# Kernel tuning notes

Measured on AMD Instinct MI355X. Metric: run time of the kernel, lower is better.

Reference implementation:

```python
import jax, jax.numpy as jnp
import numpy as np

B, T, I, H, O = 65536, 50, 2, 20, 2
P_DROP = 0.2


def setup_inputs() -> dict:
    key = jax.random.key(0)
    ks = jax.random.split(key, 8)
    s = 1.0 / np.sqrt(H)  # torch nn.RNN / nn.Linear uniform init bound
    u = lambda k, shape: jax.random.uniform(k, shape, jnp.float32, -s, s)
    x = jax.random.normal(ks[0], (B, T, I), jnp.float32)
    W_ih = u(ks[1], (H, I))
    W_hh = u(ks[2], (H, H))
    b_ih = u(ks[3], (H,))
    b_hh = u(ks[4], (H,))
    W_out = u(ks[5], (O, H))
    b_out = u(ks[6], (O,))
    # MC-dropout mask (training-mode dropout, inverted scaling), fixed for determinism
    keep = jax.random.uniform(ks[7], (B, T, H)) >= P_DROP
    drop_mask = keep.astype(jnp.float32) / (1.0 - P_DROP)
    return {"x": x, "W_ih": W_ih, "W_hh": W_hh, "b_ih": b_ih, "b_hh": b_hh,
            "W_out": W_out, "b_out": b_out, "drop_mask": drop_mask}


def reference(x, W_ih, W_hh, b_ih, b_hh, W_out, b_out, drop_mask):
    # Precompute input projection for all timesteps in one big GEMM: [B,T,H]
    xp = jnp.einsum('bti,hi->bth', x, W_ih) + b_ih + b_hh

    def step(h, xt):  # h: [B,H], xt: [B,H]
        h_new = jnp.tanh(xt + h @ W_hh.T)
        return h_new, h_new

    h0 = jnp.zeros((x.shape[0], W_hh.shape[0]), x.dtype)
    _, hs = jax.lax.scan(step, h0, jnp.swapaxes(xp, 0, 1))  # hs: [T,B,H]
    r_out = jnp.swapaxes(hs, 0, 1)  # [B,T,H]
    out = (r_out * drop_mask) @ W_out.T + b_out  # [B,T,O]
    return out
```

## Files before the change

kernel.cpp:

```cpp
#include <hip/hip_runtime.h>

#ifndef __has_builtin
#define __has_builtin(x) 0
#endif

#if __has_builtin(__builtin_amdgcn_exp2f)
#define EXP2F(x) __builtin_amdgcn_exp2f(x)
#else
#define EXP2F(x) exp2f(x)
#endif

#if __has_builtin(__builtin_amdgcn_rcpf)
#define RCPF(x) __builtin_amdgcn_rcpf(x)
#else
#define RCPF(x) (1.0f / (x))
#endif

namespace {

constexpr int kB = 65536;
constexpr int kT = 50;
constexpr int kI = 2;
constexpr int kH = 20;
constexpr int kO = 2;

__device__ __forceinline__ float fast_tanh(float v) {
    const float p = EXP2F(v * 2.8853900817779268f);
    return fmaf(-2.0f, RCPF(p + 1.0f), 1.0f);
}

#if __has_builtin(__builtin_amdgcn_mov_dpp)
template <int CTRL>
__device__ __forceinline__ float fqp(float v) {
    return __int_as_float(
        __builtin_amdgcn_mov_dpp(__float_as_int(v), CTRL, 0xF, 0xF, true));
}
#else
template <int CTRL>
__device__ __forceinline__ float fqp(float v) {
    constexpr int d = (CTRL == 0xB1) ? 1 : (CTRL == 0x4E) ? 2 : 3;
    return __shfl_xor(v, d);
}
#endif

__global__ __launch_bounds__(256)
__attribute__((amdgpu_waves_per_eu(2, 3)))
void dprnn_kernel(
    const float* __restrict__ x, const float* __restrict__ W_ih,
    const float* __restrict__ W_hh, const float* __restrict__ b_ih,
    const float* __restrict__ b_hh, const float* __restrict__ W_out,
    const float* __restrict__ b_out, const float* __restrict__ mask,
    float* __restrict__ out)
{
    const int tid = blockIdx.x * 256 + threadIdx.x;
    const int g   = tid >> 2;
    const int sub = tid & 3;
    const int gl  = threadIdx.x >> 2;

    __shared__ __align__(16) float lout[64 * kT * kO];

    float w[5][5][4];
    float wi0[5], wi1[5], bia[5], wo0[5], wo1[5];
#pragma unroll
    for (int i = 0; i < 5; ++i) {
        const int row = 4 * i + sub;
#pragma unroll
        for (int r = 0; r < 5; ++r) {
#pragma unroll
            for (int d = 0; d < 4; ++d) {
                w[i][r][d] = W_hh[row * kH + 4 * r + (sub ^ d)];
            }
        }
        wi0[i] = W_ih[row * kI + 0];
        wi1[i] = W_ih[row * kI + 1];
        bia[i] = b_ih[row] + b_hh[row];
        wo0[i] = W_out[0 * kH + row];
        wo1[i] = W_out[1 * kH + row];
    }
    const float bo0 = b_out[0];
    const float bo1 = b_out[1];

    float h[5] = {0.f, 0.f, 0.f, 0.f, 0.f};

    const float* xp = x    + (size_t)g * (kT * kI);
    const float* mp = mask + (size_t)g * (kT * kH) + sub;

    auto step = [&](const float m[5], float x0, float x1, int t) {
        float acc[5];
#pragma unroll
        for (int i = 0; i < 5; ++i)
            acc[i] = fmaf(wi0[i], x0, fmaf(wi1[i], x1, bia[i]));
#pragma unroll
        for (int r = 0; r < 5; ++r) {
            const float v0 = h[r];
            const float v1 = fqp<0xB1>(h[r]);
            const float v2 = fqp<0x4E>(h[r]);
            const float v3 = fqp<0x1B>(h[r]);
#pragma unroll
            for (int i = 0; i < 5; ++i) {
                acc[i] = fmaf(w[i][r][0], v0, acc[i]);
                acc[i] = fmaf(w[i][r][1], v1, acc[i]);
                acc[i] = fmaf(w[i][r][2], v2, acc[i]);
                acc[i] = fmaf(w[i][r][3], v3, acc[i]);
            }
        }
        float p0 = 0.f, p1 = 0.f;
#pragma unroll
        for (int i = 0; i < 5; ++i) {
            const float hn = fast_tanh(acc[i]);
            h[i] = hn;
            const float dm = hn * m[i];
            p0 = fmaf(dm, wo0[i], p0);
            p1 = fmaf(dm, wo1[i], p1);
        }
        p0 += fqp<0xB1>(p0);
        p0 += fqp<0x4E>(p0);
        p1 += fqp<0xB1>(p1);
        p1 += fqp<0x4E>(p1);
        if (sub == 0) {
            *reinterpret_cast<float2*>(&lout[gl * (kT * kO) + t * kO]) =
                make_float2(p0 + bo0, p1 + bo1);
        }
    };

    float m0[5], m1[5];
#pragma unroll
    for (int r = 0; r < 5; ++r) m0[r] = mp[0 * kH + 4 * r];
#pragma unroll
    for (int r = 0; r < 5; ++r) m1[r] = mp[1 * kH + 4 * r];
    float4 xq = *reinterpret_cast<const float4*>(xp);

    for (int tb = 0; tb < kT - 2; tb += 2) {
        float n0[5], n1[5];
        const float* mq = mp + (tb + 2) * kH;
#pragma unroll
        for (int r = 0; r < 5; ++r) n0[r] = mq[4 * r];
#pragma unroll
        for (int r = 0; r < 5; ++r) n1[r] = mq[kH + 4 * r];
        const float4 xq_n =
            *reinterpret_cast<const float4*>(xp + (tb + 2) * kI);

        step(m0, xq.x, xq.y, tb);
        step(m1, xq.z, xq.w, tb + 1);

#pragma unroll
        for (int r = 0; r < 5; ++r) { m0[r] = n0[r]; m1[r] = n1[r]; }
        xq = xq_n;
    }
    step(m0, xq.x, xq.y, kT - 2);
    step(m1, xq.z, xq.w, kT - 1);

    __syncthreads();
    const int k = threadIdx.x;
    float* ob = out + (size_t)blockIdx.x * (64 * kT * kO);
#pragma unroll
    for (int it = 0; it < 6; ++it) {
        const int idx = it * 1024 + k * 4;
        const float4 v = *reinterpret_cast<const float4*>(&lout[idx]);
        *reinterpret_cast<float4*>(ob + idx) = v;
    }
    {
        const int idx = 6144 + k;
        ob[idx] = lout[idx];
    }
}

}

extern "C" void kernel_launch(void* const* d_in, const int* in_sizes, int n_in,
                              void* d_out, int out_size, void* d_ws, size_t ws_size,
                              hipStream_t stream) {
    const float* x     = (const float*)d_in[0];
    const float* W_ih  = (const float*)d_in[1];
    const float* W_hh  = (const float*)d_in[2];
    const float* b_ih  = (const float*)d_in[3];
    const float* b_hh  = (const float*)d_in[4];
    const float* W_out = (const float*)d_in[5];
    const float* b_out = (const float*)d_in[6];
    const float* mask  = (const float*)d_in[7];
    float* out = (float*)d_out;

    const int threads = kB * 4;
    dim3 block(256);
    dim3 grid(threads / 256);
    dprnn_kernel<<<grid, block, 0, stream>>>(x, W_ih, W_hh, b_ih, b_hh,
                                             W_out, b_out, mask, out);
}
```

Before: 87.37 us.

## Stage dropout mask chunks into LDS with coalesced global_load_lds and stream outputs

```diff
diff --git a/kernel.cpp b/kernel.cpp
--- a/kernel.cpp
+++ b/kernel.cpp
@@ -14,6 +14,12 @@
 #define RCPF(x) __builtin_amdgcn_rcpf(x)
 #else
 #define RCPF(x) (1.0f / (x))
+#endif
+
+#if __has_builtin(__builtin_amdgcn_global_load_lds)
+#define USE_GLOAD_LDS 1
+#else
+#define USE_GLOAD_LDS 0
 #endif
 
 namespace {
@@ -23,6 +29,14 @@
 constexpr int kI = 2;
 constexpr int kH = 20;
 constexpr int kO = 2;
+constexpr int kCT = 5;
+constexpr int kNC = 10;
+constexpr int kGB = 64;
+
+#if USE_GLOAD_LDS
+typedef const __attribute__((address_space(1))) void* gas_ptr_t;
+typedef __attribute__((address_space(3))) void* las_ptr_t;
+#endif
 
 __device__ __forceinline__ float fast_tanh(float v) {
     const float p = EXP2F(v * 2.8853900817779268f);
@@ -52,12 +66,16 @@
     const float* __restrict__ b_out, const float* __restrict__ mask,
     float* __restrict__ out)
 {
-    const int tid = blockIdx.x * 256 + threadIdx.x;
-    const int g   = tid >> 2;
-    const int sub = tid & 3;
-    const int gl  = threadIdx.x >> 2;
-
-    __shared__ __align__(16) float lout[64 * kT * kO];
+    __shared__ __align__(16) float sm[kGB * kCT * kH + kGB * kCT * kO];
+    float* lds_m = sm;
+    float* lds_o = sm + kGB * kCT * kH;
+
+    const int tidx = threadIdx.x;
+    const int gl   = tidx >> 2;
+    const int sub  = tidx & 3;
+    const int Wv   = tidx >> 6;
+    const int lane = tidx & 63;
+    const size_t g0 = (size_t)blockIdx.x * kGB;
 
     float w[5][5][4];
     float wi0[5], wi1[5], bia[5], wo0[5], wo1[5];
@@ -65,27 +83,73 @@
     for (int i = 0; i < 5; ++i) {
         const int row = 4 * i + sub;
 #pragma unroll
-        for (int r = 0; r < 5; ++r) {
-#pragma unroll
-            for (int d = 0; d < 4; ++d) {
+        for (int r = 0; r < 5; ++r)
+#pragma unroll
+            for (int d = 0; d < 4; ++d)
                 w[i][r][d] = W_hh[row * kH + 4 * r + (sub ^ d)];
-            }
-        }
         wi0[i] = W_ih[row * kI + 0];
         wi1[i] = W_ih[row * kI + 1];
         bia[i] = b_ih[row] + b_hh[row];
-        wo0[i] = W_out[0 * kH + row];
-        wo1[i] = W_out[1 * kH + row];
+        wo0[i] = W_out[row];
+        wo1[i] = W_out[kH + row];
     }
     const float bo0 = b_out[0];
     const float bo1 = b_out[1];
 
+    const char* mask_blk = (const char*)mask + g0 * (size_t)(kT * kH * 4);
+    uint32_t srcoff[7];
+#pragma unroll
+    for (int i = 0; i < 7; ++i) {
+        const int v  = (i < 6) ? ((i * 4 + Wv) * 64 + lane) : (1536 + lane);
+        const int gv = v / 25;
+        const int wv = v - gv * 25;
+        srcoff[i] = (uint32_t)(gv * (kT * kH * 4) + wv * 16);
+    }
+
+    auto stage_mask = [&](int c) {
+        const char* src = mask_blk + c * (kCT * kH * 4);
+#if USE_GLOAD_LDS
+#pragma unroll
+        for (int i = 0; i < 6; ++i)
+            __builtin_amdgcn_global_load_lds(
+                (gas_ptr_t)(const void*)(src + srcoff[i]),
+                (las_ptr_t)(void*)((char*)sm + (i * 4 + Wv) * 1024),
+                16, 0, 0);
+        if (Wv == 0)
+            __builtin_amdgcn_global_load_lds(
+                (gas_ptr_t)(const void*)(src + srcoff[6]),
+                (las_ptr_t)(void*)((char*)sm + 24576),
+                16, 0, 0);
+#else
+        float4 t[7];
+#pragma unroll
+        for (int i = 0; i < 6; ++i)
+            t[i] = *(const float4*)(src + srcoff[i]);
+        if (Wv == 0) t[6] = *(const float4*)(src + srcoff[6]);
+#pragma unroll
+        for (int i = 0; i < 6; ++i)
+            *(float4*)((char*)sm + ((i * 4 + Wv) * 64 + lane) * 16) = t[i];
+        if (Wv == 0) *(float4*)((char*)sm + (1536 + lane) * 16) = t[6];
+#endif
+    };
+
+    const float* xg = x + (g0 + gl) * (kT * kI);
+    float2 xA[kCT];
+    auto load_x = [&](int c) {
+#pragma unroll
+        for (int j = 0; j < kCT; ++j)
+            xA[j] = *(const float2*)(xg + c * (kCT * kI) + j * kI);
+    };
+
     float h[5] = {0.f, 0.f, 0.f, 0.f, 0.f};
-
-    const float* xp = x    + (size_t)g * (kT * kI);
-    const float* mp = mask + (size_t)g * (kT * kH) + sub;
-
-    auto step = [&](const float m[5], float x0, float x1, int t) {
+    const int mbase = gl * (kCT * kH) + sub;
+
+    auto step = [&](int j) {
+        float m[5];
+#pragma unroll
+        for (int r = 0; r < 5; ++r)
+            m[r] = lds_m[mbase + j * kH + 4 * r];
+        const float x0 = xA[j].x, x1 = xA[j].y;
         float acc[5];
 #pragma unroll
         for (int i = 0; i < 5; ++i)
@@ -117,51 +181,40 @@
         p0 += fqp<0x4E>(p0);
         p1 += fqp<0xB1>(p1);
         p1 += fqp<0x4E>(p1);
-        if (sub == 0) {
-            *reinterpret_cast<float2*>(&lout[gl * (kT * kO) + t * kO]) =
+        if (sub == 0)
+            *(float2*)&lds_o[gl * (kCT * kO) + j * kO] =
                 make_float2(p0 + bo0, p1 + bo1);
-        }
-    };
-
-    float m0[5], m1[5];
-#pragma unroll
-    for (int r = 0; r < 5; ++r) m0[r] = mp[0 * kH + 4 * r];
-#pragma unroll
-    for (int r = 0; r < 5; ++r) m1[r] = mp[1 * kH + 4 * r];
-    float4 xq = *reinterpret_cast<const float4*>(xp);
-
-    for (int tb = 0; tb < kT - 2; tb += 2) {
-        float n0[5], n1[5];
-        const float* mq = mp + (tb + 2) * kH;
-#pragma unroll
-        for (int r = 0; r < 5; ++r) n0[r] = mq[4 * r];
-#pragma unroll
-        for (int r = 0; r < 5; ++r) n1[r] = mq[kH + 4 * r];
-        const float4 xq_n =
-            *reinterpret_cast<const float4*>(xp + (tb + 2) * kI);
-
-        step(m0, xq.x, xq.y, tb);
-        step(m1, xq.z, xq.w, tb + 1);
-
-#pragma unroll
-        for (int r = 0; r < 5; ++r) { m0[r] = n0[r]; m1[r] = n1[r]; }
-        xq = xq_n;
-    }
-    step(m0, xq.x, xq.y, kT - 2);
-    step(m1, xq.z, xq.w, kT - 1);
-
+    };
+
+    auto flush_out = [&](int c) {
+        {
+            const int j  = tidx;
+            const int gq = j / 5, wq = j - gq * 5;
+            const float2 v = *(const float2*)&lds_o[gq * (kCT * kO) + wq * kO];
+            *(float2*)(out + (g0 + gq) * (kT * kO) + c * (kCT * kO) + wq * kO) = v;
+        }
+        if (tidx < 64) {
+            const int j  = 256 + tidx;
+            const int gq = j / 5, wq = j - gq * 5;
+            const float2 v = *(const float2*)&lds_o[gq * (kCT * kO) + wq * kO];
+            *(float2*)(out + (g0 + gq) * (kT * kO) + c * (kCT * kO) + wq * kO) = v;
+        }
+    };
+
+    stage_mask(0);
+    load_x(0);
     __syncthreads();
-    const int k = threadIdx.x;
-    float* ob = out + (size_t)blockIdx.x * (64 * kT * kO);
-#pragma unroll
-    for (int it = 0; it < 6; ++it) {
-        const int idx = it * 1024 + k * 4;
-        const float4 v = *reinterpret_cast<const float4*>(&lout[idx]);
-        *reinterpret_cast<float4*>(ob + idx) = v;
-    }
-    {
-        const int idx = 6144 + k;
-        ob[idx] = lout[idx];
+
+    for (int c = 0; c < kNC; ++c) {
+#pragma unroll
+        for (int j = 0; j < kCT; ++j) step(j);
+        __syncthreads();
+        if (c + 1 < kNC) {
+            stage_mask(c + 1);
+            load_x(c + 1);
+        }
+        flush_out(c);
+        __syncthreads();
     }
 }
 
@@ -180,9 +233,8 @@
     const float* mask  = (const float*)d_in[7];
     float* out = (float*)d_out;
 
-    const int threads = kB * 4;
     dim3 block(256);
-    dim3 grid(threads / 256);
+    dim3 grid(kB / kGB);
     dprnn_kernel<<<grid, block, 0, stream>>>(x, W_ih, W_hh, b_ih, b_hh,
                                              W_out, b_out, mask, out);
 }
```

Result: slower. 106.0 us (+21.3%).

## Stage dropout mask through LDS in coalesced 4-step chunks with prefetch

Applied to the files above, without the earlier changes.

```diff
diff --git a/kernel.cpp b/kernel.cpp
--- a/kernel.cpp
+++ b/kernel.cpp
@@ -23,6 +23,10 @@
 constexpr int kI = 2;
 constexpr int kH = 20;
 constexpr int kO = 2;
+constexpr int kCT = 4;
+constexpr int kNC = 12;
+constexpr int kQS = 84;
+constexpr int kGB = 64;
 
 __device__ __forceinline__ float fast_tanh(float v) {
     const float p = EXP2F(v * 2.8853900817779268f);
@@ -44,7 +48,7 @@
 #endif
 
 __global__ __launch_bounds__(256)
-__attribute__((amdgpu_waves_per_eu(2, 3)))
+__attribute__((amdgpu_waves_per_eu(2)))
 void dprnn_kernel(
     const float* __restrict__ x, const float* __restrict__ W_ih,
     const float* __restrict__ W_hh, const float* __restrict__ b_ih,
@@ -52,12 +56,14 @@
     const float* __restrict__ b_out, const float* __restrict__ mask,
     float* __restrict__ out)
 {
-    const int tid = blockIdx.x * 256 + threadIdx.x;
-    const int g   = tid >> 2;
-    const int sub = tid & 3;
-    const int gl  = threadIdx.x >> 2;
-
-    __shared__ __align__(16) float lout[64 * kT * kO];
+    __shared__ __align__(16) float sm[kGB * kQS + kGB * kT * kO];
+    float* lds_m = sm;
+    float* lds_o = sm + kGB * kQS;
+
+    const int tidx = threadIdx.x;
+    const int gl   = tidx >> 2;
+    const int sub  = tidx & 3;
+    const size_t g = (size_t)blockIdx.x * kGB + gl;
 
     float w[5][5][4];
     float wi0[5], wi1[5], bia[5], wo0[5], wo1[5];
@@ -65,27 +71,45 @@
     for (int i = 0; i < 5; ++i) {
         const int row = 4 * i + sub;
 #pragma unroll
-        for (int r = 0; r < 5; ++r) {
-#pragma unroll
-            for (int d = 0; d < 4; ++d) {
+        for (int r = 0; r < 5; ++r)
+#pragma unroll
+            for (int d = 0; d < 4; ++d)
                 w[i][r][d] = W_hh[row * kH + 4 * r + (sub ^ d)];
-            }
-        }
         wi0[i] = W_ih[row * kI + 0];
         wi1[i] = W_ih[row * kI + 1];
         bia[i] = b_ih[row] + b_hh[row];
-        wo0[i] = W_out[0 * kH + row];
-        wo1[i] = W_out[1 * kH + row];
+        wo0[i] = W_out[row];
+        wo1[i] = W_out[kH + row];
     }
     const float bo0 = b_out[0];
     const float bo1 = b_out[1];
 
+    const float* msrc = mask + g * (kT * kH) + sub * 20;
+    const float* mrow = mask + g * (kT * kH) + sub;
+    const float* xsrc = x + g * (kT * kI);
+    const int wbase = gl * kQS + sub * 20;
+    const int rbase = gl * kQS + sub;
+
+    float4 f[5];
+    float4 xF[2], xA[2];
+    float m48[5], m49[5];
+
+    auto load_chunk = [&](int c) {
+#pragma unroll
+        for (int j = 0; j < 5; ++j)
+            f[j] = *(const float4*)(msrc + c * 80 + 4 * j);
+        xF[0] = *(const float4*)(xsrc + c * 8);
+        xF[1] = *(const float4*)(xsrc + c * 8 + 4);
+    };
+    auto write_chunk = [&]() {
+#pragma unroll
+        for (int j = 0; j < 5; ++j)
+            *(float4*)&lds_m[wbase + 4 * j] = f[j];
+    };
+
     float h[5] = {0.f, 0.f, 0.f, 0.f, 0.f};
 
-    const float* xp = x    + (size_t)g * (kT * kI);
-    const float* mp = mask + (size_t)g * (kT * kH) + sub;
-
-    auto step = [&](const float m[5], float x0, float x1, int t) {
+    auto core = [&](const float m[5], float x0, float x1, int t) {
         float acc[5];
 #pragma unroll
         for (int i = 0; i < 5; ++i)
@@ -117,51 +141,59 @@
         p0 += fqp<0x4E>(p0);
         p1 += fqp<0xB1>(p1);
         p1 += fqp<0x4E>(p1);
-        if (sub == 0) {
-            *reinterpret_cast<float2*>(&lout[gl * (kT * kO) + t * kO]) =
+        if (sub == 0)
+            *(float2*)&lds_o[gl * (kT * kO) + t * kO] =
                 make_float2(p0 + bo0, p1 + bo1);
-        }
     };
 
-    float m0[5], m1[5];
-#pragma unroll
-    for (int r = 0; r < 5; ++r) m0[r] = mp[0 * kH + 4 * r];
-#pragma unroll
-    for (int r = 0; r < 5; ++r) m1[r] = mp[1 * kH + 4 * r];
-    float4 xq = *reinterpret_cast<const float4*>(xp);
-
-    for (int tb = 0; tb < kT - 2; tb += 2) {
-        float n0[5], n1[5];
-        const float* mq = mp + (tb + 2) * kH;
-#pragma unroll
-        for (int r = 0; r < 5; ++r) n0[r] = mq[4 * r];
-#pragma unroll
-        for (int r = 0; r < 5; ++r) n1[r] = mq[kH + 4 * r];
-        const float4 xq_n =
-            *reinterpret_cast<const float4*>(xp + (tb + 2) * kI);
-
-        step(m0, xq.x, xq.y, tb);
-        step(m1, xq.z, xq.w, tb + 1);
-
-#pragma unroll
-        for (int r = 0; r < 5; ++r) { m0[r] = n0[r]; m1[r] = n1[r]; }
-        xq = xq_n;
-    }
-    step(m0, xq.x, xq.y, kT - 2);
-    step(m1, xq.z, xq.w, kT - 1);
+    load_chunk(0);
+    write_chunk();
+    xA[0] = xF[0]; xA[1] = xF[1];
+    load_chunk(1);
+
+#pragma unroll 1
+    for (int c = 0; c < kNC; ++c) {
+#pragma unroll
+        for (int s = 0; s < kCT; ++s) {
+            float m[5];
+#pragma unroll
+            for (int r = 0; r < 5; ++r)
+                m[r] = lds_m[rbase + s * kH + 4 * r];
+            const float x0 = (s == 0) ? xA[0].x : (s == 1) ? xA[0].z
+                            : (s == 2) ? xA[1].x : xA[1].z;
+            const float x1 = (s == 0) ? xA[0].y : (s == 1) ? xA[0].w
+                            : (s == 2) ? xA[1].y : xA[1].w;
+            core(m, x0, x1, c * kCT + s);
+        }
+        if (c < kNC - 1) {
+            write_chunk();
+            xA[0] = xF[0]; xA[1] = xF[1];
+            if (c < kNC - 2) {
+                load_chunk(c + 2);
+            } else {
+#pragma unroll
+                for (int r = 0; r < 5; ++r) {
+                    m48[r] = mrow[48 * kH + 4 * r];
+                    m49[r] = mrow[49 * kH + 4 * r];
+                }
+                xF[0] = *(const float4*)(xsrc + 96);
+            }
+        }
+    }
+    core(m48, xF[0].x, xF[0].y, 48);
+    core(m49, xF[0].z, xF[0].w, 49);
 
     __syncthreads();
-    const int k = threadIdx.x;
-    float* ob = out + (size_t)blockIdx.x * (64 * kT * kO);
+    float* ob = out + (size_t)blockIdx.x * (kGB * kT * kO);
 #pragma unroll
     for (int it = 0; it < 6; ++it) {
-        const int idx = it * 1024 + k * 4;
-        const float4 v = *reinterpret_cast<const float4*>(&lout[idx]);
-        *reinterpret_cast<float4*>(ob + idx) = v;
+        const int idx = it * 1024 + tidx * 4;
+        const float4 v = *(const float4*)&lds_o[idx];
+        *(float4*)(ob + idx) = v;
     }
     {
-        const int idx = 6144 + k;
-        ob[idx] = lout[idx];
+        const int idx = 6144 + tidx;
+        ob[idx] = lds_o[idx];
     }
 }
 
@@ -180,9 +212,8 @@
     const float* mask  = (const float*)d_in[7];
     float* out = (float*)d_out;
 
-    const int threads = kB * 4;
     dim3 block(256);
-    dim3 grid(threads / 256);
+    dim3 grid(kB / kGB);
     dprnn_kernel<<<grid, block, 0, stream>>>(x, W_ih, W_hh, b_ih, b_hh,
                                              W_out, b_out, mask, out);
 }
```

After: 145.7 us. +66.7%, slower.
